# Kernel optimization log

Measured on AMD Instinct MI355X. Metric: run time of the kernel, lower is better.

Reference implementation:

```python
import jax, jax.numpy as jnp
import numpy as np

B, S, E, H = 2, 2048, 1024, 16
DH = E // H  # 64
EPS = 1e-5


def layer_norm(x, g, b):
    mu = jnp.mean(x, axis=-1, keepdims=True)
    var = jnp.mean(jnp.square(x - mu), axis=-1, keepdims=True)
    return (x - mu) * jax.lax.rsqrt(var + EPS) * g + b


def setup_inputs() -> dict:
    key = jax.random.key(0)
    ks = jax.random.split(key, 12)
    s = lambda fan_in: 1.0 / np.sqrt(fan_in)
    return {
        "x": jax.random.normal(ks[0], (B, S, E), dtype=jnp.float32),
        "ln1_g": jnp.ones((E,), jnp.float32),
        "ln1_b": jnp.zeros((E,), jnp.float32),
        # per-head projections, batched over head axis: [H, E, DH]
        "Wq": jax.random.uniform(ks[1], (H, E, DH), jnp.float32, -s(E), s(E)),
        "Wk": jax.random.uniform(ks[2], (H, E, DH), jnp.float32, -s(E), s(E)),
        "Wv": jax.random.uniform(ks[3], (H, E, DH), jnp.float32, -s(E), s(E)),
        "Wo": jax.random.uniform(ks[4], (H * DH, E), jnp.float32, -s(H * DH), s(H * DH)),
        "bo": jax.random.uniform(ks[5], (E,), jnp.float32, -s(H * DH), s(H * DH)),
        "ln2_g": jnp.ones((E,), jnp.float32),
        "ln2_b": jnp.zeros((E,), jnp.float32),
        "W1": jax.random.uniform(ks[6], (E, 4 * E), jnp.float32, -s(E), s(E)),
        "b1": jax.random.uniform(ks[7], (4 * E,), jnp.float32, -s(E), s(E)),
        "W2": jax.random.uniform(ks[8], (4 * E, E), jnp.float32, -s(4 * E), s(4 * E)),
        "b2": jax.random.uniform(ks[9], (E,), jnp.float32, -s(4 * E), s(4 * E)),
    }


def reference(x, ln1_g, ln1_b, Wq, Wk, Wv, Wo, bo, ln2_g, ln2_b, W1, b1, W2, b2):
    b, s, e = x.shape
    # --- multi-head attention (pre-LN) ---
    h = layer_norm(x, ln1_g, ln1_b)
    q = jnp.einsum("bse,hed->bhsd", h, Wq)
    k = jnp.einsum("bse,hed->bhsd", h, Wk)
    v = jnp.einsum("bse,hed->bhsd", h, Wv)
    # NOTE: original scales by channel**-0.5 (embed_size), not head_size
    scores = jnp.einsum("bhsd,bhtd->bhst", q, k) * (e ** -0.5)
    causal = jnp.tril(jnp.ones((s, s), dtype=bool))
    scores = jnp.where(causal, scores, -jnp.inf)
    attn = jax.nn.softmax(scores, axis=-1)  # dropout is identity in eval
    out = jnp.einsum("bhst,bhtd->bhsd", attn, v)
    out = out.transpose(0, 2, 1, 3).reshape(b, s, -1)  # concat heads: [B,S,H*DH]
    x = x + out @ Wo + bo
    # --- feed-forward (pre-LN) ---
    h2 = layer_norm(x, ln2_g, ln2_b)
    ff = jax.nn.relu(h2 @ W1 + b1) @ W2 + b2
    return x + ff
```

## Files before the change

### kernel.cpp

```cpp
#include <hip/hip_runtime.h>


typedef __bf16 bf16_t;
typedef __attribute__((ext_vector_type(8))) __bf16 bf16x8;
typedef __attribute__((ext_vector_type(4))) __bf16 bf16x4;
typedef __attribute__((ext_vector_type(4))) float f32x4;

#define B_DIM 2
#define S_DIM 2048
#define E_DIM 1024
#define H_DIM 16
#define DH_DIM 64

#define GLD16(gp, lp) __builtin_amdgcn_global_load_lds( \
    (const __attribute__((address_space(1))) void*)(gp), \
    (__attribute__((address_space(3))) void*)(lp), 16, 0, 0)

#define Q_SCALE 0.0450842120f

__global__ __launch_bounds__(256) void ln_kernel(
    const float* __restrict__ x, const float* __restrict__ g,
    const float* __restrict__ bv, bf16_t* __restrict__ out)
{
  const int row = blockIdx.x;
  const int t = threadIdx.x;
  const float* xr = x + (size_t)row * E_DIM;
  float4 v = *(const float4*)&xr[t * 4];
  float s  = v.x + v.y + v.z + v.w;
  float s2 = v.x*v.x + v.y*v.y + v.z*v.z + v.w*v.w;
#pragma unroll
  for (int m = 1; m < 64; m <<= 1) {
    s  += __shfl_xor(s,  m, 64);
    s2 += __shfl_xor(s2, m, 64);
  }
  __shared__ float red[8];
  const int wid = t >> 6, lane = t & 63;
  if (lane == 0) { red[wid] = s; red[4 + wid] = s2; }
  __syncthreads();
  s  = red[0] + red[1] + red[2] + red[3];
  s2 = red[4] + red[5] + red[6] + red[7];
  const float mu  = s * (1.f / E_DIM);
  const float var = s2 * (1.f / E_DIM) - mu * mu;
  const float rs  = rsqrtf(var + 1e-5f);
  float4 gg = *(const float4*)&g[t * 4];
  float4 bb = *(const float4*)&bv[t * 4];
  bf16x4 o;
  o[0] = (bf16_t)((v.x - mu) * rs * gg.x + bb.x);
  o[1] = (bf16_t)((v.y - mu) * rs * gg.y + bb.y);
  o[2] = (bf16_t)((v.z - mu) * rs * gg.z + bb.z);
  o[3] = (bf16_t)((v.w - mu) * rs * gg.w + bb.w);
  *(bf16x4*)&out[(size_t)row * E_DIM + t * 4] = o;
}

__global__ __launch_bounds__(256) void reduce2_ln(
    const float* __restrict__ p, const float* __restrict__ bo,
    const float* __restrict__ x, const float* __restrict__ g,
    const float* __restrict__ bv, float* __restrict__ xmid, bf16_t* __restrict__ h2)
{
  const int row = blockIdx.x;
  const int t = threadIdx.x;
  const size_t off = (size_t)row * E_DIM + t * 4;
  float4 a  = *(const float4*)&p[off];
  float4 b4 = *(const float4*)&p[(size_t)4096 * E_DIM + off];
  float4 xr = *(const float4*)&x[off];
  float4 bo4 = *(const float4*)&bo[t * 4];
  float4 v;
  v.x = a.x + b4.x + xr.x + bo4.x;
  v.y = a.y + b4.y + xr.y + bo4.y;
  v.z = a.z + b4.z + xr.z + bo4.z;
  v.w = a.w + b4.w + xr.w + bo4.w;
  *(float4*)&xmid[off] = v;
  float s  = v.x + v.y + v.z + v.w;
  float s2 = v.x*v.x + v.y*v.y + v.z*v.z + v.w*v.w;
#pragma unroll
  for (int m = 1; m < 64; m <<= 1) {
    s  += __shfl_xor(s,  m, 64);
    s2 += __shfl_xor(s2, m, 64);
  }
  __shared__ float red[8];
  const int wid = t >> 6, lane = t & 63;
  if (lane == 0) { red[wid] = s; red[4 + wid] = s2; }
  __syncthreads();
  s  = red[0] + red[1] + red[2] + red[3];
  s2 = red[4] + red[5] + red[6] + red[7];
  const float mu  = s * (1.f / E_DIM);
  const float var = s2 * (1.f / E_DIM) - mu * mu;
  const float rs  = rsqrtf(var + 1e-5f);
  float4 gg = *(const float4*)&g[t * 4];
  float4 bb = *(const float4*)&bv[t * 4];
  bf16x4 o;
  o[0] = (bf16_t)((v.x - mu) * rs * gg.x + bb.x);
  o[1] = (bf16_t)((v.y - mu) * rs * gg.y + bb.y);
  o[2] = (bf16_t)((v.z - mu) * rs * gg.z + bb.z);
  o[3] = (bf16_t)((v.w - mu) * rs * gg.w + bb.w);
  *(bf16x4*)&h2[off] = o;
}

__global__ __launch_bounds__(256) void reduce4(
    const bf16_t* __restrict__ p0, const bf16_t* __restrict__ p1,
    const bf16_t* __restrict__ p2, const bf16_t* __restrict__ p3,
    const float* __restrict__ b2, const float* __restrict__ xm,
    float* __restrict__ out)
{
  const int row = blockIdx.x;
  const int t = threadIdx.x;
  const size_t off = (size_t)row * E_DIM + t * 4;
  bf16x4 a0 = *(const bf16x4*)&p0[off];
  bf16x4 a1 = *(const bf16x4*)&p1[off];
  bf16x4 a2 = *(const bf16x4*)&p2[off];
  bf16x4 a3 = *(const bf16x4*)&p3[off];
  float4 xr = *(const float4*)&xm[off];
  float4 bb = *(const float4*)&b2[t * 4];
  float4 o;
  o.x = (float)a0[0] + (float)a1[0] + (float)a2[0] + (float)a3[0] + xr.x + bb.x;
  o.y = (float)a0[1] + (float)a1[1] + (float)a2[1] + (float)a3[1] + xr.y + bb.y;
  o.z = (float)a0[2] + (float)a1[2] + (float)a2[2] + (float)a3[2] + xr.z + bb.z;
  o.w = (float)a0[3] + (float)a1[3] + (float)a2[3] + (float)a3[3] + xr.w + bb.w;
  *(float4*)&out[off] = o;
}

__global__ __launch_bounds__(256) void transpose_cast(
    const float* __restrict__ src, bf16_t* __restrict__ dst, int R, int C)
{
  __shared__ float tile[64][65];
  const int c0 = blockIdx.x * 64, r0 = blockIdx.y * 64;
  const int t = threadIdx.x;
  const int rr = t >> 2;
#pragma unroll
  for (int u = 0; u < 4; u++) {
    const int cc = (t & 3) * 4 + u * 16;
    float4 f = *(const float4*)&src[(size_t)(r0 + rr) * C + c0 + cc];
    tile[rr][cc + 0] = f.x; tile[rr][cc + 1] = f.y;
    tile[rr][cc + 2] = f.z; tile[rr][cc + 3] = f.w;
  }
  __syncthreads();
  const int oc = t >> 2;
#pragma unroll
  for (int u = 0; u < 4; u++) {
    const int orr = (t & 3) * 4 + u * 16;
    bf16x4 w;
    w[0] = (bf16_t)tile[orr + 0][oc];
    w[1] = (bf16_t)tile[orr + 1][oc];
    w[2] = (bf16_t)tile[orr + 2][oc];
    w[3] = (bf16_t)tile[orr + 3][oc];
    *(bf16x4*)&dst[(size_t)(c0 + oc) * R + r0 + orr] = w;
  }
}

__global__ __launch_bounds__(256) void qkv_transpose(
    const float* __restrict__ Wq, const float* __restrict__ Wk,
    const float* __restrict__ Wv, bf16_t* __restrict__ dstT)
{
  const int m = blockIdx.y >> 4, h = blockIdx.y & 15;
  const float* src = (m == 0 ? Wq : (m == 1 ? Wk : Wv)) + (size_t)h * E_DIM * DH_DIM;
  const int e0 = blockIdx.x * 64;
  __shared__ float tile[64][65];
  const int t = threadIdx.x;
  const int rr = t >> 2;
#pragma unroll
  for (int u = 0; u < 4; u++) {
    const int cc = (t & 3) * 4 + u * 16;
    float4 f = *(const float4*)&src[(size_t)(e0 + rr) * DH_DIM + cc];
    tile[rr][cc + 0] = f.x; tile[rr][cc + 1] = f.y;
    tile[rr][cc + 2] = f.z; tile[rr][cc + 3] = f.w;
  }
  __syncthreads();
  const int oc = t >> 2;
  const size_t drow = (size_t)(m * 1024 + h * 64 + oc) * E_DIM;
#pragma unroll
  for (int u = 0; u < 4; u++) {
    const int orr = (t & 3) * 4 + u * 16;
    bf16x4 w;
    w[0] = (bf16_t)tile[orr + 0][oc];
    w[1] = (bf16_t)tile[orr + 1][oc];
    w[2] = (bf16_t)tile[orr + 2][oc];
    w[3] = (bf16_t)tile[orr + 3][oc];
    *(bf16x4*)&dstT[drow + e0 + orr] = w;
  }
}

constexpr int EPI_QKV = 0, EPI_BIAS_RELU = 2, EPI_PART_F32 = 3, EPI_PART_B16 = 4;


template <int EPI>
__global__ __launch_bounds__(256) void gemm128_kernel(
    const bf16_t* __restrict__ A, const bf16_t* __restrict__ Bt,
    int M, int N, int Kst, int Klen,
    const float* __restrict__ bias,
    float* __restrict__ outF, bf16_t* __restrict__ outB,
    bf16_t* __restrict__ qo, bf16_t* __restrict__ ko, bf16_t* __restrict__ vo)
{
  __shared__ bf16_t As[3][128 * 32];
  __shared__ bf16_t Bs[3][128 * 32];
  const int gx = gridDim.x;
  const int nwg = gx * gridDim.y;
  int id = blockIdx.y * gx + blockIdx.x;
  id = (id & 7) * (nwg >> 3) + (id >> 3);
  const int m0 = (id % gx) * 128, n0 = (id / gx) * 128;
  const int sp = blockIdx.z;
  A  += (size_t)sp * Klen;
  Bt += (size_t)sp * Klen;

  const int tid = threadIdx.x, lane = tid & 63, wid = tid >> 6;
  const int wr = wid >> 1, wc = wid & 1;
  const int lr = lane & 15, lg = lane >> 4;
  const int halfr = lr >> 1;
  const int sl16 = (((lr & 1) * 4 + lg) ^ halfr) * 16;
  const int baseA = (wr * 32 + halfr) * 128 + sl16;
  const int baseB = (wc * 32 + halfr) * 128 + sl16;

  auto stage = [&](int kt, int buf) {
#pragma unroll
    for (int p = 0; p < 2; p++) {
      const int L = p * 256 + tid;
      const int row2 = L >> 3;
      const int s = (L & 7) ^ (row2 & 7);
      const int r = row2 * 2 + (s >> 2);
      const int u = s & 3;
      char* lb = (char*)&As[buf][0] + (size_t)(p * 256 + wid * 64) * 16;
      char* lbB = (char*)&Bs[buf][0] + (size_t)(p * 256 + wid * 64) * 16;
      GLD16(A  + (size_t)(m0 + r) * Kst + kt * 32 + u * 8, lb);
      GLD16(Bt + (size_t)(n0 + r) * Kst + kt * 32 + u * 8, lbB);
    }
  };

  const f32x4 z4 = {0.f, 0.f, 0.f, 0.f};
  f32x4 acc[4][4];
#pragma unroll
  for (int i = 0; i < 4; i++)
#pragma unroll
    for (int j = 0; j < 4; j++) acc[i][j] = z4;

  const int NT = Klen / 32;
  stage(0, 0);
  stage(1, 1);
  for (int T = 0; T < NT; ++T) {
    const int b = T % 3;
    if (T + 1 < NT) asm volatile("s_waitcnt vmcnt(4)" ::: "memory");
    else            asm volatile("s_waitcnt vmcnt(0)" ::: "memory");
    __builtin_amdgcn_s_barrier();
    if (T + 2 < NT) stage(T + 2, (T + 2) % 3);
    __builtin_amdgcn_sched_barrier(0);

    bf16x8 af[4], bfr[4];
#pragma unroll
    for (int j = 0; j < 4; j++)
      bfr[j] = *(const bf16x8*)((const char*)&Bs[b][0] + baseB + j * 1024);
#pragma unroll
    for (int i = 0; i < 4; i++)
      af[i] = *(const bf16x8*)((const char*)&As[b][0] + baseA + i * 1024);
    __builtin_amdgcn_s_setprio(1);
#pragma unroll
    for (int i = 0; i < 4; i++)
#pragma unroll
      for (int j = 0; j < 4; j++)
        acc[i][j] = __builtin_amdgcn_mfma_f32_16x16x32_bf16(af[i], bfr[j], acc[i][j], 0, 0, 0);
    __builtin_amdgcn_s_setprio(0);
  }

#pragma unroll
  for (int i = 0; i < 4; i++) {
#pragma unroll
    for (int j = 0; j < 4; j++) {
#pragma unroll
      for (int r = 0; r < 4; r++) {
        const int m = m0 + wr * 64 + i * 16 + lg * 4 + r;
        const int n = n0 + wc * 64 + j * 16 + lr;
        const float val = acc[i][j][r];
        if constexpr (EPI == EPI_QKV) {
          const int tsel = n >> 10, h = (n >> 6) & 15, d = n & 63;
          const int b_ = m >> 11, s_ = m & 2047;
          if (tsel == 0)
            qo[((size_t)((b_ * H_DIM + h) * S_DIM + s_)) * DH_DIM + d] = (bf16_t)(val * Q_SCALE);
          else if (tsel == 1)
            ko[((size_t)((b_ * H_DIM + h) * S_DIM + s_)) * DH_DIM + d] = (bf16_t)val;
          else
            vo[((size_t)((b_ * H_DIM + h) * DH_DIM + d)) * S_DIM + s_] = (bf16_t)val;
        } else if constexpr (EPI == EPI_BIAS_RELU) {
          const float u = val + bias[n];
          outB[(size_t)m * N + n] = (bf16_t)(u > 0.f ? u : 0.f);
        } else if constexpr (EPI == EPI_PART_F32) {
          outF[(size_t)sp * M * N + (size_t)m * N + n] = val;
        } else {
          bf16_t* o = sp == 0 ? outB : sp == 1 ? qo : sp == 2 ? ko : vo;
          o[(size_t)m * N + n] = (bf16_t)val;
        }
      }
    }
  }
}

__global__ __launch_bounds__(256) void attn_kernel(
    const bf16_t* __restrict__ Q, const bf16_t* __restrict__ K,
    const bf16_t* __restrict__ Vt, bf16_t* __restrict__ O,
    bf16_t* __restrict__ Opart, float* __restrict__ mpart, float* __restrict__ lpart)
{
  __shared__ bf16_t Ks[2][64 * 64];
  __shared__ bf16_t Vs[2][64 * 64];
  __shared__ bf16_t Ps[4][2][16 * 64];

  const int nwg = 40 * gridDim.y;
  int id = blockIdx.y * 40 + blockIdx.x;
  id = (id & 7) * (nwg >> 3) + (id >> 3);
  const int bx = id % 40, bh = id / 40;

  int q2, sp, ns;
  if (bx < 4)       { q2 = bx;                      sp = 0;          ns = 1; }
  else if (bx < 12) { const int u = bx - 4;  q2 = 4 + (u >> 1);  sp = u & 1;  ns = 2; }
  else if (bx < 24) { const int u = bx - 12; const int q3 = u / 3;
                      q2 = 8 + q3;                  sp = u - q3 * 3; ns = 3; }
  else              { const int u = bx - 24; q2 = 12 + (u >> 2); sp = u & 3;  ns = 4; }
  const int n2 = 2 * q2 + 2;
  const int lo = (sp * n2) / ns, hi = ((sp + 1) * n2) / ns;

  const int tid = threadIdx.x;
  const int wid = tid >> 6, lane = tid & 63;
  const int lr = lane & 15, lg = lane >> 4;
  const int q0w = q2 * 128 + wid * 32;

  const bf16_t* Qp = Q  + (size_t)bh * S_DIM * DH_DIM;
  const bf16_t* Kp = K  + (size_t)bh * S_DIM * DH_DIM;
  const bf16_t* Vp = Vt + (size_t)bh * DH_DIM * S_DIM;

  bf16x8 bq0[2], bq1[2];
#pragma unroll
  for (int c = 0; c < 2; c++) {
    bq0[c] = *(const bf16x8*)&Qp[(size_t)(q0w + lr) * DH_DIM + c * 32 + lg * 8];
    bq1[c] = *(const bf16x8*)&Qp[(size_t)(q0w + 16 + lr) * DH_DIM + c * 32 + lg * 8];
  }

  const f32x4 z4 = {0.f, 0.f, 0.f, 0.f};
  f32x4 Ot0[4], Ot1[4];
#pragma unroll
  for (int dt = 0; dt < 4; dt++) { Ot0[dt] = z4; Ot1[dt] = z4; }
  float mrow0 = -1e30f, lrow0 = 0.f;
  float mrow1 = -1e30f, lrow1 = 0.f;

  const int ktr = wid * 8 + (lane >> 3);
  const int ksc = lane & 7;

  auto stageKV = [&](int t0, int buf) {
#pragma unroll
    for (int p = 0; p < 2; p++) {
      const int tr = p * 32 + ktr;
      GLD16(Kp + (size_t)(t0 + tr) * DH_DIM + (ksc ^ (tr & 7)) * 8,
            &Ks[buf][(p * 32 + wid * 8) * 64]);
      GLD16(Vp + (size_t)tr * S_DIM + t0 + (ksc ^ (tr & 7)) * 8,
            &Vs[buf][(p * 32 + wid * 8) * 64]);
    }
  };

  stageKV(lo * 64, 0);

  for (int tc = lo; tc < hi; ++tc) {
    const int cur = (tc - lo) & 1;
    __syncthreads();
    if (tc + 1 < hi) stageKV((tc + 1) * 64, cur ^ 1);

    const int t0 = tc * 64;
    f32x4 s0[4], s1[4];
    __builtin_amdgcn_s_setprio(1);
#pragma unroll
    for (int j = 0; j < 4; j++) {
      f32x4 a = z4, b = z4;
      const int t = j * 16 + lr;
#pragma unroll
      for (int c = 0; c < 2; c++) {
        const int kbyte = t * 128 + (((c * 4 + lg) * 16) ^ ((t & 7) << 4));
        bf16x8 ak = *(const bf16x8*)((const char*)&Ks[cur][0] + kbyte);
        a = __builtin_amdgcn_mfma_f32_16x16x32_bf16(ak, bq0[c], a, 0, 0, 0);
        b = __builtin_amdgcn_mfma_f32_16x16x32_bf16(ak, bq1[c], b, 0, 0, 0);
      }
      s0[j] = a; s1[j] = b;
    }
    __builtin_amdgcn_s_setprio(0);
    if (tc >= 2 * q2) {
#pragma unroll
      for (int j = 0; j < 4; j++)
#pragma unroll
        for (int r = 0; r < 4; r++) {
          const int tg = t0 + j * 16 + lg * 4 + r;
          if (tg > q0w + lr)      s0[j][r] = -1e30f;
          if (tg > q0w + 16 + lr) s1[j][r] = -1e30f;
        }
    }
    {
      float mj[4];
#pragma unroll
      for (int j = 0; j < 4; j++)
        mj[j] = fmaxf(fmaxf(s0[j][0], s0[j][1]), fmaxf(s0[j][2], s0[j][3]));
      float tmax = fmaxf(fmaxf(mj[0], mj[1]), fmaxf(mj[2], mj[3]));
      tmax = fmaxf(tmax, __shfl_xor(tmax, 16, 64));
      tmax = fmaxf(tmax, __shfl_xor(tmax, 32, 64));
      if (!__all(tmax <= mrow0 + 8.f)) {
        const float mnew = fmaxf(mrow0, tmax);
        const float fsc = __builtin_exp2f(mrow0 - mnew);
        mrow0 = mnew; lrow0 *= fsc;
#pragma unroll
        for (int dt = 0; dt < 4; dt++)
#pragma unroll
          for (int r = 0; r < 4; r++) Ot0[dt][r] *= fsc;
      }
      float sj[4];
#pragma unroll
      for (int j = 0; j < 4; j++) {
#pragma unroll
        for (int r = 0; r < 4; r++) s0[j][r] = __builtin_exp2f(s0[j][r] - mrow0);
        sj[j] = (s0[j][0] + s0[j][1]) + (s0[j][2] + s0[j][3]);
      }
      float tsum = (sj[0] + sj[1]) + (sj[2] + sj[3]);
      tsum += __shfl_xor(tsum, 16, 64);
      tsum += __shfl_xor(tsum, 32, 64);
      lrow0 += tsum;
#pragma unroll
      for (int j = 0; j < 4; j++) {
        bf16x4 w;
#pragma unroll
        for (int r = 0; r < 4; r++) w[r] = (bf16_t)s0[j][r];
        const int pbyte = lr * 128 + ((j * 32 + lg * 8) ^ ((lr & 7) << 4));
        *(bf16x4*)((char*)&Ps[wid][0][0] + pbyte) = w;
      }
    }
    {
      float mj[4];
#pragma unroll
      for (int j = 0; j < 4; j++)
        mj[j] = fmaxf(fmaxf(s1[j][0], s1[j][1]), fmaxf(s1[j][2], s1[j][3]));
      float tmax = fmaxf(fmaxf(mj[0], mj[1]), fmaxf(mj[2], mj[3]));
      tmax = fmaxf(tmax, __shfl_xor(tmax, 16, 64));
      tmax = fmaxf(tmax, __shfl_xor(tmax, 32, 64));
      if (!__all(tmax <= mrow1 + 8.f)) {
        const float mnew = fmaxf(mrow1, tmax);
        const float fsc = __builtin_exp2f(mrow1 - mnew);
        mrow1 = mnew; lrow1 *= fsc;
#pragma unroll
        for (int dt = 0; dt < 4; dt++)
#pragma unroll
          for (int r = 0; r < 4; r++) Ot1[dt][r] *= fsc;
      }
      float sj[4];
#pragma unroll
      for (int j = 0; j < 4; j++) {
#pragma unroll
        for (int r = 0; r < 4; r++) s1[j][r] = __builtin_exp2f(s1[j][r] - mrow1);
        sj[j] = (s1[j][0] + s1[j][1]) + (s1[j][2] + s1[j][3]);
      }
      float tsum = (sj[0] + sj[1]) + (sj[2] + sj[3]);
      tsum += __shfl_xor(tsum, 16, 64);
      tsum += __shfl_xor(tsum, 32, 64);
      lrow1 += tsum;
#pragma unroll
      for (int j = 0; j < 4; j++) {
        bf16x4 w;
#pragma unroll
        for (int r = 0; r < 4; r++) w[r] = (bf16_t)s1[j][r];
        const int pbyte = lr * 128 + ((j * 32 + lg * 8) ^ ((lr & 7) << 4));
        *(bf16x4*)((char*)&Ps[wid][1][0] + pbyte) = w;
      }
    }

    __builtin_amdgcn_s_setprio(1);
#pragma unroll
    for (int c = 0; c < 2; c++) {
      const int abyte = lr * 128 + ((c * 64 + lg * 16) ^ ((lr & 7) << 4));
      bf16x8 pa0 = *(const bf16x8*)((const char*)&Ps[wid][0][0] + abyte);
      bf16x8 pa1 = *(const bf16x8*)((const char*)&Ps[wid][1][0] + abyte);
#pragma unroll
      for (int dt = 0; dt < 4; dt++) {
        const int d = dt * 16 + lr;
        const int vbyte = d * 128 + (((c * 4 + lg) * 16) ^ ((d & 7) << 4));
        bf16x8 bv = *(const bf16x8*)((const char*)&Vs[cur][0] + vbyte);
        Ot0[dt] = __builtin_amdgcn_mfma_f32_16x16x32_bf16(bv, pa0, Ot0[dt], 0, 0, 0);
        Ot1[dt] = __builtin_amdgcn_mfma_f32_16x16x32_bf16(bv, pa1, Ot1[dt], 0, 0, 0);
      }
    }
    __builtin_amdgcn_s_setprio(0);
  }

  if (ns == 1) {
    const int b = bh >> 4, h = bh & 15;
    {
      const float linv = 1.f / lrow0;
      const size_t base = ((size_t)(b * S_DIM + q0w + lr)) * E_DIM + h * DH_DIM;
#pragma unroll
      for (int dt = 0; dt < 4; dt++) {
        bf16x4 w;
#pragma unroll
        for (int r = 0; r < 4; r++) w[r] = (bf16_t)(Ot0[dt][r] * linv);
        *(bf16x4*)&O[base + dt * 16 + lg * 4] = w;
      }
    }
    {
      const float linv = 1.f / lrow1;
      const size_t base = ((size_t)(b * S_DIM + q0w + 16 + lr)) * E_DIM + h * DH_DIM;
#pragma unroll
      for (int dt = 0; dt < 4; dt++) {
        bf16x4 w;
#pragma unroll
        for (int r = 0; r < 4; r++) w[r] = (bf16_t)(Ot1[dt][r] * linv);
        *(bf16x4*)&O[base + dt * 16 + lg * 4] = w;
      }
    }
  } else {
    const int sbase = (q2 < 8) ? 4 + 2 * (q2 - 4)
                     : (q2 < 12) ? 12 + 3 * (q2 - 8) : 24 + 4 * (q2 - 12);
    const int psl = bh * 36 + (sbase - 4) + sp;
    bf16_t* Ob = Opart + (size_t)psl * 128 * 64;
    const int row0 = wid * 32 + lr, row1 = row0 + 16;
#pragma unroll
    for (int dt = 0; dt < 4; dt++) {
      bf16x4 w0, w1;
#pragma unroll
      for (int r = 0; r < 4; r++) { w0[r] = (bf16_t)Ot0[dt][r]; w1[r] = (bf16_t)Ot1[dt][r]; }
      *(bf16x4*)&Ob[row0 * 64 + dt * 16 + lg * 4] = w0;
      *(bf16x4*)&Ob[row1 * 64 + dt * 16 + lg * 4] = w1;
    }
    if (lg == 0) {
      mpart[psl * 128 + row0] = mrow0;
      lpart[psl * 128 + row0] = lrow0;
      mpart[psl * 128 + row1] = mrow1;
      lpart[psl * 128 + row1] = lrow1;
    }
  }
}

__global__ __launch_bounds__(256) void attn_combine(
    const bf16_t* __restrict__ Opart, const float* __restrict__ mpart,
    const float* __restrict__ lpart, bf16_t* __restrict__ O)
{
  const int q2 = 4 + (blockIdx.x >> 1);
  const int half = blockIdx.x & 1;
  const int bh = blockIdx.y;
  const int ns = (q2 < 8) ? 2 : (q2 < 12) ? 3 : 4;
  const int sbase = (q2 < 8) ? 4 + 2 * (q2 - 4)
                   : (q2 < 12) ? 12 + 3 * (q2 - 8) : 24 + 4 * (q2 - 12);
  const int psl0 = bh * 36 + (sbase - 4);
  const int tid = threadIdx.x;
  const int q = tid >> 2, d0 = (tid & 3) * 16;
  const int row = half * 64 + q;

  float M = -1e30f;
  for (int s = 0; s < ns; s++) M = fmaxf(M, mpart[(psl0 + s) * 128 + row]);
  float L = 0.f;
  float acc[16];
#pragma unroll
  for (int j = 0; j < 16; j++) acc[j] = 0.f;
  for (int s = 0; s < ns; s++) {
    const float w = __builtin_exp2f(mpart[(psl0 + s) * 128 + row] - M);
    L += w * lpart[(psl0 + s) * 128 + row];
    const bf16_t* Ob = Opart + ((size_t)(psl0 + s) * 128 + row) * 64 + d0;
    bf16x8 o0 = *(const bf16x8*)Ob;
    bf16x8 o1 = *(const bf16x8*)(Ob + 8);
#pragma unroll
    for (int j = 0; j < 8; j++) { acc[j] += w * (float)o0[j]; acc[8 + j] += w * (float)o1[j]; }
  }
  const float inv = 1.f / L;
  const int b = bh >> 4, h = bh & 15;
  const int srow = q2 * 128 + row;
  bf16_t* out = O + ((size_t)(b * S_DIM + srow)) * E_DIM + h * DH_DIM + d0;
  bf16x8 w0, w1;
#pragma unroll
  for (int j = 0; j < 8; j++) { w0[j] = (bf16_t)(acc[j] * inv); w1[j] = (bf16_t)(acc[8 + j] * inv); }
  *(bf16x8*)out = w0;
  *(bf16x8*)(out + 8) = w1;
}

extern "C" void kernel_launch(void* const* d_in, const int* in_sizes, int n_in,
                              void* d_out, int out_size, void* d_ws, size_t ws_size,
                              hipStream_t stream)
{
  const float* x    = (const float*)d_in[0];
  const float* ln1g = (const float*)d_in[1];
  const float* ln1b = (const float*)d_in[2];
  const float* Wq   = (const float*)d_in[3];
  const float* Wk   = (const float*)d_in[4];
  const float* Wv   = (const float*)d_in[5];
  const float* Wo   = (const float*)d_in[6];
  const float* bo   = (const float*)d_in[7];
  const float* ln2g = (const float*)d_in[8];
  const float* ln2b = (const float*)d_in[9];
  const float* W1   = (const float*)d_in[10];
  const float* b1   = (const float*)d_in[11];
  const float* W2   = (const float*)d_in[12];
  const float* b2   = (const float*)d_in[13];

  char* ws = (char*)d_ws;
  bf16_t* WqkvT = (bf16_t*)(ws + 0);
  bf16_t* WoT   = (bf16_t*)(ws + 6291456);
  bf16_t* W1T   = (bf16_t*)(ws + 8388608);
  bf16_t* W2T   = (bf16_t*)(ws + 16777216);
  bf16_t* h1    = (bf16_t*)(ws + 25165824);
  bf16_t* qb    = (bf16_t*)(ws + 33554432);
  bf16_t* kb    = (bf16_t*)(ws + 41943040);
  bf16_t* vb    = (bf16_t*)(ws + 50331648);
  bf16_t* attnb = (bf16_t*)(ws + 58720256);
  float*  xmid  = (float* )(ws + 67108864);
  bf16_t* h2    = (bf16_t*)(ws + 83886080);
  bf16_t* ff1   = (bf16_t*)(ws + 25165824);
  bf16_t* Opart = (bf16_t*)(ws + 67108864);
  float*  mpart = (float* )(ws + 25165824);
  float*  lpart = (float* )(ws + 25755648);
  float*  po    = (float* )(ws + 25165824);
  bf16_t* pf0   = (bf16_t*)(ws + 0);
  bf16_t* pf1   = (bf16_t*)(ws + 8388608);
  bf16_t* pf2   = (bf16_t*)(ws + 58720256);
  bf16_t* pf3   = (bf16_t*)(ws + 83886080);

  qkv_transpose<<<dim3(16, 48), 256, 0, stream>>>(Wq, Wk, Wv, WqkvT);
  transpose_cast<<<dim3(16, 16), 256, 0, stream>>>(Wo, WoT, 1024, 1024);
  transpose_cast<<<dim3(64, 16), 256, 0, stream>>>(W1, W1T, 1024, 4096);
  transpose_cast<<<dim3(16, 64), 256, 0, stream>>>(W2, W2T, 4096, 1024);

  ln_kernel<<<4096, 256, 0, stream>>>(x, ln1g, ln1b, h1);
  gemm128_kernel<EPI_QKV><<<dim3(32, 24, 1), 256, 0, stream>>>(
      h1, WqkvT, 4096, 3072, 1024, 1024, nullptr,
      nullptr, nullptr, qb, kb, vb);
  attn_kernel<<<dim3(40, 32), 256, 0, stream>>>(qb, kb, vb, attnb, Opart, mpart, lpart);
  attn_combine<<<dim3(24, 32), 256, 0, stream>>>(Opart, mpart, lpart, attnb);
  gemm128_kernel<EPI_PART_F32><<<dim3(32, 8, 2), 256, 0, stream>>>(
      attnb, WoT, 4096, 1024, 1024, 512, nullptr,
      po, nullptr, nullptr, nullptr, nullptr);
  reduce2_ln<<<4096, 256, 0, stream>>>(po, bo, x, ln2g, ln2b, xmid, h2);
  gemm128_kernel<EPI_BIAS_RELU><<<dim3(32, 32, 1), 256, 0, stream>>>(
      h2, W1T, 4096, 4096, 1024, 1024, b1,
      nullptr, ff1, nullptr, nullptr, nullptr);
  gemm128_kernel<EPI_PART_B16><<<dim3(32, 8, 4), 256, 0, stream>>>(
      ff1, W2T, 4096, 1024, 4096, 1024, nullptr,
      nullptr, pf0, pf1, pf2, pf3);
  reduce4<<<4096, 256, 0, stream>>>(pf0, pf1, pf2, pf3, b2, xmid, (float*)d_out);

  (void)in_sizes; (void)n_in; (void)out_size; (void)ws_size;
}
```

Measured before the change: 298.2 us.

## Use 256x256-tile GEMM for FFN, double-buffer GEMMs, bf16 Wo partials

Adds a 512-thread GEMM kernel with 256x256 output tiles and uses it for both FFN matmuls, raising data reuse per workgroup. The 128-tile GEMM drops from triple to double buffering, waiting for all loads each iteration, which lowers LDS use but exposes more load latency. The Wo split-K partials are now stored in bf16 instead of fp32, halving that traffic at some cost in precision. The larger kernel also uses fewer workgroups (256 for W1, 256 for W2) and more accumulator registers per thread.

```diff
diff --git a/kernel.cpp b/kernel.cpp
--- a/kernel.cpp
+++ b/kernel.cpp
@@ -53,22 +53,23 @@
 }
 
 __global__ __launch_bounds__(256) void reduce2_ln(
-    const float* __restrict__ p, const float* __restrict__ bo,
-    const float* __restrict__ x, const float* __restrict__ g,
-    const float* __restrict__ bv, float* __restrict__ xmid, bf16_t* __restrict__ h2)
+    const bf16_t* __restrict__ p0, const bf16_t* __restrict__ p1,
+    const float* __restrict__ bo, const float* __restrict__ x,
+    const float* __restrict__ g, const float* __restrict__ bv,
+    float* __restrict__ xmid, bf16_t* __restrict__ h2)
 {
   const int row = blockIdx.x;
   const int t = threadIdx.x;
   const size_t off = (size_t)row * E_DIM + t * 4;
-  float4 a  = *(const float4*)&p[off];
-  float4 b4 = *(const float4*)&p[(size_t)4096 * E_DIM + off];
+  bf16x4 a = *(const bf16x4*)&p0[off];
+  bf16x4 b4 = *(const bf16x4*)&p1[off];
   float4 xr = *(const float4*)&x[off];
   float4 bo4 = *(const float4*)&bo[t * 4];
   float4 v;
-  v.x = a.x + b4.x + xr.x + bo4.x;
-  v.y = a.y + b4.y + xr.y + bo4.y;
-  v.z = a.z + b4.z + xr.z + bo4.z;
-  v.w = a.w + b4.w + xr.w + bo4.w;
+  v.x = (float)a[0] + (float)b4[0] + xr.x + bo4.x;
+  v.y = (float)a[1] + (float)b4[1] + xr.y + bo4.y;
+  v.z = (float)a[2] + (float)b4[2] + xr.z + bo4.z;
+  v.w = (float)a[3] + (float)b4[3] + xr.w + bo4.w;
   *(float4*)&xmid[off] = v;
   float s  = v.x + v.y + v.z + v.w;
   float s2 = v.x*v.x + v.y*v.y + v.z*v.z + v.w*v.w;
@@ -190,8 +191,8 @@
     float* __restrict__ outF, bf16_t* __restrict__ outB,
     bf16_t* __restrict__ qo, bf16_t* __restrict__ ko, bf16_t* __restrict__ vo)
 {
-  __shared__ bf16_t As[3][128 * 32];
-  __shared__ bf16_t Bs[3][128 * 32];
+  __shared__ bf16_t As[2][128 * 32];
+  __shared__ bf16_t Bs[2][128 * 32];
   const int gx = gridDim.x;
   const int nwg = gx * gridDim.y;
   int id = blockIdx.y * gx + blockIdx.x;
@@ -233,13 +234,11 @@
 
   const int NT = Klen / 32;
   stage(0, 0);
-  stage(1, 1);
   for (int T = 0; T < NT; ++T) {
-    const int b = T % 3;
-    if (T + 1 < NT) asm volatile("s_waitcnt vmcnt(4)" ::: "memory");
-    else            asm volatile("s_waitcnt vmcnt(0)" ::: "memory");
+    const int b = T & 1;
+    asm volatile("s_waitcnt vmcnt(0)" ::: "memory");
     __builtin_amdgcn_s_barrier();
-    if (T + 2 < NT) stage(T + 2, (T + 2) % 3);
+    if (T + 1 < NT) stage(T + 1, b ^ 1);
     __builtin_amdgcn_sched_barrier(0);
 
     bf16x8 af[4], bfr[4];
@@ -290,6 +289,102 @@
   }
 }
 
+template <int EPI>
+__global__ __launch_bounds__(512, 2) void gemm256_kernel(
+    const bf16_t* __restrict__ A, const bf16_t* __restrict__ Bt,
+    int M, int N, int Kst, int Klen,
+    const float* __restrict__ bias,
+    float* __restrict__ outF, bf16_t* __restrict__ outB,
+    bf16_t* __restrict__ qo, bf16_t* __restrict__ ko, bf16_t* __restrict__ vo)
+{
+  __shared__ bf16_t As[2][256 * 32];
+  __shared__ bf16_t Bs[2][256 * 32];
+  const int gx = gridDim.x;
+  const int nwg = gx * gridDim.y;
+  int id = blockIdx.y * gx + blockIdx.x;
+  id = (id & 7) * (nwg >> 3) + (id >> 3);
+  const int m0 = (id % gx) * 256, n0 = (id / gx) * 256;
+  const int sp = blockIdx.z;
+  A  += (size_t)sp * Klen;
+  Bt += (size_t)sp * Klen;
+
+  const int tid = threadIdx.x, lane = tid & 63, wid = tid >> 6;
+  const int wm = wid >> 2, wn = wid & 3;
+  const int lr = lane & 15, lg = lane >> 4;
+  const int halfr = lr >> 1;
+  const int sl16 = (((lr & 1) * 4 + lg) ^ halfr) * 16;
+  const int baseA = (wm * 64 + halfr) * 128 + sl16;
+  const int baseB = (wn * 32 + halfr) * 128 + sl16;
+
+  auto stage = [&](int kt, int buf) {
+#pragma unroll
+    for (int p = 0; p < 2; p++) {
+      const int L = p * 512 + tid;
+      const int row2 = L >> 3;
+      const int s = (L & 7) ^ (row2 & 7);
+      const int r = row2 * 2 + (s >> 2);
+      const int u = s & 3;
+      char* lb = (char*)&As[buf][0] + (size_t)(p * 512 + wid * 64) * 16;
+      char* lbB = (char*)&Bs[buf][0] + (size_t)(p * 512 + wid * 64) * 16;
+      GLD16(A  + (size_t)(m0 + r) * Kst + kt * 32 + u * 8, lb);
+      GLD16(Bt + (size_t)(n0 + r) * Kst + kt * 32 + u * 8, lbB);
+    }
+  };
+
+  const f32x4 z4 = {0.f, 0.f, 0.f, 0.f};
+  f32x4 acc[8][4];
+#pragma unroll
+  for (int i = 0; i < 8; i++)
+#pragma unroll
+    for (int j = 0; j < 4; j++) acc[i][j] = z4;
+
+  const int NT = Klen / 32;
+  stage(0, 0);
+  for (int T = 0; T < NT; ++T) {
+    const int b = T & 1;
+    asm volatile("s_waitcnt vmcnt(0)" ::: "memory");
+    __builtin_amdgcn_s_barrier();
+    if (T + 1 < NT) stage(T + 1, b ^ 1);
+    __builtin_amdgcn_sched_barrier(0);
+
+    bf16x8 bfr[4];
+#pragma unroll
+    for (int j = 0; j < 4; j++)
+      bfr[j] = *(const bf16x8*)((const char*)&Bs[b][0] + baseB + j * 1024);
+    __builtin_amdgcn_s_setprio(1);
+#pragma unroll
+    for (int i = 0; i < 8; i++) {
+      bf16x8 af = *(const bf16x8*)((const char*)&As[b][0] + baseA + i * 1024);
+#pragma unroll
+      for (int j = 0; j < 4; j++)
+        acc[i][j] = __builtin_amdgcn_mfma_f32_16x16x32_bf16(af, bfr[j], acc[i][j], 0, 0, 0);
+    }
+    __builtin_amdgcn_s_setprio(0);
+  }
+
+#pragma unroll
+  for (int i = 0; i < 8; i++) {
+#pragma unroll
+    for (int j = 0; j < 4; j++) {
+#pragma unroll
+      for (int r = 0; r < 4; r++) {
+        const int m = m0 + wm * 128 + i * 16 + lg * 4 + r;
+        const int n = n0 + wn * 64 + j * 16 + lr;
+        const float val = acc[i][j][r];
+        if constexpr (EPI == EPI_BIAS_RELU) {
+          const float u = val + bias[n];
+          outB[(size_t)m * N + n] = (bf16_t)(u > 0.f ? u : 0.f);
+        } else if constexpr (EPI == EPI_PART_F32) {
+          outF[(size_t)sp * M * N + (size_t)m * N + n] = val;
+        } else if constexpr (EPI == EPI_PART_B16) {
+          bf16_t* o = sp == 0 ? outB : sp == 1 ? qo : sp == 2 ? ko : vo;
+          o[(size_t)m * N + n] = (bf16_t)val;
+        }
+      }
+    }
+  }
+}
+
 __global__ __launch_bounds__(256) void attn_kernel(
     const bf16_t* __restrict__ Q, const bf16_t* __restrict__ K,
     const bf16_t* __restrict__ Vt, bf16_t* __restrict__ O,
@@ -600,7 +695,8 @@
   bf16_t* Opart = (bf16_t*)(ws + 67108864);
   float*  mpart = (float* )(ws + 25165824);
   float*  lpart = (float* )(ws + 25755648);
-  float*  po    = (float* )(ws + 25165824);
+  bf16_t* po0   = (bf16_t*)(ws + 25165824);
+  bf16_t* po1   = (bf16_t*)(ws + 33554432);
   bf16_t* pf0   = (bf16_t*)(ws + 0);
   bf16_t* pf1   = (bf16_t*)(ws + 8388608);
   bf16_t* pf2   = (bf16_t*)(ws + 58720256);
@@ -617,14 +713,14 @@
       nullptr, nullptr, qb, kb, vb);
   attn_kernel<<<dim3(40, 32), 256, 0, stream>>>(qb, kb, vb, attnb, Opart, mpart, lpart);
   attn_combine<<<dim3(24, 32), 256, 0, stream>>>(Opart, mpart, lpart, attnb);
-  gemm128_kernel<EPI_PART_F32><<<dim3(32, 8, 2), 256, 0, stream>>>(
+  gemm128_kernel<EPI_PART_B16><<<dim3(32, 8, 2), 256, 0, stream>>>(
       attnb, WoT, 4096, 1024, 1024, 512, nullptr,
-      po, nullptr, nullptr, nullptr, nullptr);
-  reduce2_ln<<<4096, 256, 0, stream>>>(po, bo, x, ln2g, ln2b, xmid, h2);
-  gemm128_kernel<EPI_BIAS_RELU><<<dim3(32, 32, 1), 256, 0, stream>>>(
+      nullptr, po0, po1, nullptr, nullptr);
+  reduce2_ln<<<4096, 256, 0, stream>>>(po0, po1, bo, x, ln2g, ln2b, xmid, h2);
+  gemm256_kernel<EPI_BIAS_RELU><<<dim3(16, 16, 1), 512, 0, stream>>>(
       h2, W1T, 4096, 4096, 1024, 1024, b1,
       nullptr, ff1, nullptr, nullptr, nullptr);
-  gemm128_kernel<EPI_PART_B16><<<dim3(32, 8, 4), 256, 0, stream>>>(
+  gemm256_kernel<EPI_PART_B16><<<dim3(16, 4, 4), 512, 0, stream>>>(
       ff1, W2T, 4096, 1024, 4096, 1024, nullptr,
       nullptr, pf0, pf1, pf2, pf3);
   reduce4<<<4096, 256, 0, stream>>>(pf0, pf1, pf2, pf3, b2, xmid, (float*)d_out);
```

Result: faster. 281.5 us (-5.6%).
